# Kernel optimization log

Measured on AMD Instinct MI355X. Metric: run time of the kernel, lower is better.

## Reference

```python
import jax, jax.numpy as jnp
import numpy as np

E, T, D, H = 8, 2048, 1024, 4096  # experts, tokens/expert, model_dim, hidden_size


def setup_inputs() -> dict:
    key = jax.random.key(0)
    k_x, k_w1, k_w2 = jax.random.split(key, 3)
    x = jax.random.normal(k_x, (E, T, D), dtype=jnp.float32)
    fc1_w = jax.random.normal(k_w1, (E, D, H), dtype=jnp.float32) * 0.001
    fc2_w = jax.random.normal(k_w2, (E, H, D), dtype=jnp.float32) * 0.001
    fc1_b = jnp.zeros((E, 1, H), dtype=jnp.float32)
    fc2_b = jnp.zeros((E, 1, D), dtype=jnp.float32)
    return {"x": x, "fc1_w": fc1_w, "fc1_b": fc1_b, "fc2_w": fc2_w, "fc2_b": fc2_b}


def reference(x, fc1_w, fc1_b, fc2_w, fc2_b):
    # batched expert FFN: bmm + bias -> relu -> bmm + bias
    y = jnp.einsum("etd,edh->eth", x, fc1_w) + fc1_b  # [E, T, H]
    y = jax.nn.relu(y)
    y = jnp.einsum("eth,ehd->etd", y, fc2_w) + fc2_b  # [E, T, D]
    return y
```

## Files before the change

kernel.cpp:

```cpp
#include <hip/hip_runtime.h>
#include <hip/hip_bf16.h>
#include <stdint.h>


using frag8 = __attribute__((ext_vector_type(8))) short;
using f32x4 = __attribute__((ext_vector_type(4))) float;

constexpr int E = 8, T = 2048, D = 1024, H = 4096;
constexpr int BM = 256, BN = 256, BK = 64;

__device__ __forceinline__ ushort f2bf(float f) {
    union { float f; uint32_t u; } v; v.f = f;
    return (ushort)((v.u + 0x7FFFu + ((v.u >> 16) & 1u)) >> 16);
}

__device__ __forceinline__ void load16_to_lds(const void* g, void* l) {
    __builtin_amdgcn_global_load_lds(
        (const __attribute__((address_space(1))) uint32_t*)g,
        (__attribute__((address_space(3))) uint32_t*)l, 16, 0, 0);
}


__global__ __launch_bounds__(256) void cvt_bf16_kernel(
    const float* __restrict__ in, ushort* __restrict__ out) {
    const size_t i = ((size_t)blockIdx.x * 256 + threadIdx.x) * 4;
    const float4 v = *(const float4*)(in + i);
    ushort4 o;
    o.x = f2bf(v.x); o.y = f2bf(v.y); o.z = f2bf(v.z); o.w = f2bf(v.w);
    *(ushort4*)(out + i) = o;
}

__global__ __launch_bounds__(256) void transpose_cvt_kernel(
    const float* __restrict__ in, ushort* __restrict__ out, int K, int N) {
    __shared__ __align__(16) ushort tile[64][72];
    const int e = blockIdx.z;
    const int k0 = blockIdx.y * 64, n0 = blockIdx.x * 64;
    const float* ie = in + (size_t)e * K * N + (size_t)k0 * N + n0;
    ushort* oe = out + (size_t)e * N * K + (size_t)n0 * K + k0;
    const int t = threadIdx.x;
    const int lk = t >> 2;
    const int ln = (t & 3) * 16;
#pragma unroll
    for (int v = 0; v < 4; ++v) {
        const float4 f = *(const float4*)(ie + (size_t)lk * N + ln + v * 4);
        tile[ln + v * 4 + 0][lk] = f2bf(f.x);
        tile[ln + v * 4 + 1][lk] = f2bf(f.y);
        tile[ln + v * 4 + 2][lk] = f2bf(f.z);
        tile[ln + v * 4 + 3][lk] = f2bf(f.w);
    }
    __syncthreads();
    const int on = t >> 2;
    const int ok = (t & 3) * 16;
#pragma unroll
    for (int v = 0; v < 2; ++v)
        *(frag8*)(oe + (size_t)on * K + ok + v * 8) = *(const frag8*)&tile[on][ok + v * 8];
}

template <bool RELU_BF16>
__global__ __launch_bounds__(512, 2) void gemm256_kernel(
    const ushort* __restrict__ A, const ushort* __restrict__ Bm,
    const float* __restrict__ bias, void* __restrict__ Cout,
    const int K, const int N) {
    __shared__ __align__(16) char lds[131072];

    const int bid = blockIdx.x;
    const int e = bid & 7;
    const int s = bid >> 3;
    const int m0 = (s & 7) * BM;
    const int n0 = (s >> 3) * BN;

    const ushort* Ae = A + (size_t)e * T * K + (size_t)m0 * K;
    const ushort* Be = Bm + (size_t)e * N * K + (size_t)n0 * K;

    const int tid = threadIdx.x;
    const int lane = tid & 63;
    const int wave = tid >> 6;
    const int wm = wave >> 2;
    const int wn = wave & 3;
    const int col = lane & 15;
    const int quad = lane >> 4;

    const int scc = (lane & 7) ^ (lane >> 3);
    const int srow = wave * 8 + (lane >> 3);
    const ushort* gA0 = Ae + (size_t)srow * K + scc * 8;
    const ushort* gB0 = Be + (size_t)srow * K + scc * 8;
    const int ldsA0 = wave * 1024;
    const int ldsB0 = 32768 + wave * 1024;

    const int swz0 = ((quad ^ (col & 7)) << 4);
    const int swz1 = swz0 ^ 64;
    const int aRow = (wm * 128 + col) * 128;
    const int bRow = (wn * 64 + col) * 128;

    const int NT = K / BK;

#define STAGE_A(p, h, kk) do {                                          \
        const ushort* g_ = gA0 + (size_t)(h) * 128 * K + (kk);          \
        char* l_ = lds + (p) * 65536 + ldsA0 + (h) * 16384;             \
        load16_to_lds(g_, l_);                                          \
        load16_to_lds(g_ + (size_t)64 * K, l_ + 8192);                  \
    } while (0)
#define STAGE_B(p, h, kk) do {                                          \
        const ushort* g_ = gB0 + (size_t)(h) * 128 * K + (kk);          \
        char* l_ = lds + (p) * 65536 + ldsB0 + (h) * 16384;             \
        load16_to_lds(g_, l_);                                          \
        load16_to_lds(g_ + (size_t)64 * K, l_ + 8192);                  \
    } while (0)
#define MFMA(a, b, c) __builtin_amdgcn_mfma_f32_16x16x32_bf16((a), (b), (c), 0, 0, 0)

    f32x4 acc[8][4] = {};
    frag8 A0f[8], A1f[8], Bf[4];

    STAGE_A(0, 0, 0); STAGE_A(0, 1, 0);
    STAGE_B(0, 0, 0); STAGE_B(0, 1, 0);
    STAGE_A(1, 0, BK); STAGE_A(1, 1, BK);
    asm volatile("s_waitcnt vmcnt(4)" ::: "memory");
    __builtin_amdgcn_s_barrier();
    __builtin_amdgcn_sched_barrier(0);

    for (int u = 0; u < NT; ++u) {
        const int p = u & 1, pn = p ^ 1;
        const int kB = (u + 1) * BK;
        const int kA = (u + 2) * BK;
        const bool stB = (u + 1 < NT), stA = (u + 2 < NT);
        const char* aT = lds + p * 65536 + aRow;
        const char* bT = lds + p * 65536 + 32768 + bRow;

#pragma unroll
        for (int i = 0; i < 4; ++i) {
            A0f[i * 2 + 0] = *(const frag8*)(aT + i * 2048 + swz0);
            A0f[i * 2 + 1] = *(const frag8*)(aT + i * 2048 + swz1);
        }
#pragma unroll
        for (int j = 0; j < 2; ++j) {
            Bf[j * 2 + 0] = *(const frag8*)(bT + j * 2048 + swz0);
            Bf[j * 2 + 1] = *(const frag8*)(bT + j * 2048 + swz1);
        }
        if (stB) STAGE_B(pn, 0, kB);
        __builtin_amdgcn_s_barrier();
        asm volatile("s_waitcnt lgkmcnt(0)" ::: "memory");
        __builtin_amdgcn_sched_barrier(0);
        __builtin_amdgcn_s_setprio(1);
#pragma unroll
        for (int i = 0; i < 4; ++i)
#pragma unroll
            for (int j = 0; j < 2; ++j) {
                acc[i][j] = MFMA(A0f[i * 2 + 0], Bf[j * 2 + 0], acc[i][j]);
                acc[i][j] = MFMA(A0f[i * 2 + 1], Bf[j * 2 + 1], acc[i][j]);
            }
        __builtin_amdgcn_s_setprio(0);
        __builtin_amdgcn_s_barrier();
        __builtin_amdgcn_sched_barrier(0);

#pragma unroll
        for (int i = 0; i < 4; ++i) {
            A1f[i * 2 + 0] = *(const frag8*)(aT + 8192 + i * 2048 + swz0);
            A1f[i * 2 + 1] = *(const frag8*)(aT + 8192 + i * 2048 + swz1);
        }
        if (stB) STAGE_B(pn, 1, kB);
        __builtin_amdgcn_s_barrier();
        asm volatile("s_waitcnt lgkmcnt(0)" ::: "memory");
        __builtin_amdgcn_sched_barrier(0);
        __builtin_amdgcn_s_setprio(1);
#pragma unroll
        for (int i = 0; i < 4; ++i)
#pragma unroll
            for (int j = 0; j < 2; ++j) {
                acc[4 + i][j] = MFMA(A1f[i * 2 + 0], Bf[j * 2 + 0], acc[4 + i][j]);
                acc[4 + i][j] = MFMA(A1f[i * 2 + 1], Bf[j * 2 + 1], acc[4 + i][j]);
            }
        __builtin_amdgcn_s_setprio(0);
        __builtin_amdgcn_s_barrier();
        __builtin_amdgcn_sched_barrier(0);

#pragma unroll
        for (int j = 0; j < 2; ++j) {
            Bf[j * 2 + 0] = *(const frag8*)(bT + 4096 + j * 2048 + swz0);
            Bf[j * 2 + 1] = *(const frag8*)(bT + 4096 + j * 2048 + swz1);
        }
        if (stA) STAGE_A(p, 0, kA);
        __builtin_amdgcn_s_barrier();
        asm volatile("s_waitcnt lgkmcnt(0)" ::: "memory");
        __builtin_amdgcn_sched_barrier(0);
        __builtin_amdgcn_s_setprio(1);
#pragma unroll
        for (int i = 0; i < 4; ++i)
#pragma unroll
            for (int j = 0; j < 2; ++j) {
                acc[4 + i][2 + j] = MFMA(A1f[i * 2 + 0], Bf[j * 2 + 0], acc[4 + i][2 + j]);
                acc[4 + i][2 + j] = MFMA(A1f[i * 2 + 1], Bf[j * 2 + 1], acc[4 + i][2 + j]);
            }
        __builtin_amdgcn_s_setprio(0);
        __builtin_amdgcn_s_barrier();
        __builtin_amdgcn_sched_barrier(0);

        if (stA) STAGE_A(p, 1, kA);
        __builtin_amdgcn_s_barrier();
        __builtin_amdgcn_sched_barrier(0);
        __builtin_amdgcn_s_setprio(1);
#pragma unroll
        for (int i = 0; i < 4; ++i)
#pragma unroll
            for (int j = 0; j < 2; ++j) {
                acc[i][2 + j] = MFMA(A0f[i * 2 + 0], Bf[j * 2 + 0], acc[i][2 + j]);
                acc[i][2 + j] = MFMA(A0f[i * 2 + 1], Bf[j * 2 + 1], acc[i][2 + j]);
            }
        __builtin_amdgcn_s_setprio(0);
        if (stA) {
            asm volatile("s_waitcnt vmcnt(4)" ::: "memory");
        } else if (stB) {
            asm volatile("s_waitcnt vmcnt(0)" ::: "memory");
        }
        __builtin_amdgcn_s_barrier();
        __builtin_amdgcn_sched_barrier(0);
    }

    const float* be = bias + (size_t)e * N;
#pragma unroll
    for (int j = 0; j < 4; ++j) {
        const int nn = n0 + wn * 64 + j * 16 + col;
        const float bv = be[nn];
#pragma unroll
        for (int i = 0; i < 8; ++i) {
            const int mb = m0 + wm * 128 + i * 16 + quad * 4;
#pragma unroll
            for (int r = 0; r < 4; ++r) {
                float v = acc[i][j][r] + bv;
                if (RELU_BF16) {
                    v = v > 0.f ? v : 0.f;
                    ((ushort*)Cout)[(size_t)e * T * N + (size_t)(mb + r) * N + nn] = f2bf(v);
                } else {
                    ((float*)Cout)[(size_t)e * T * N + (size_t)(mb + r) * N + nn] = v;
                }
            }
        }
    }
#undef STAGE_A
#undef STAGE_B
#undef MFMA
}


constexpr int FBM = 128, FBN = 128, FBK = 32;
constexpr int FLDK = FBK + 16;

__global__ __launch_bounds__(256) void fb_gemm1_kernel(
    const float* __restrict__ x, const float* __restrict__ w1,
    const float* __restrict__ b1, ushort* __restrict__ y1) {
    __shared__ __align__(16) ushort As[FBM * FLDK];
    __shared__ __align__(16) ushort Bs[FBN * FLDK];
    const int e = blockIdx.z, m0 = blockIdx.y * FBM, n0 = blockIdx.x * FBN;
    const float* xa = x + (size_t)e * T * D + (size_t)m0 * D;
    const float* wb = w1 + (size_t)e * D * H;
    const int tid = threadIdx.x, lane = tid & 63, wave = tid >> 6;
    const int waveM = (wave >> 1) * 64, waveN = (wave & 1) * 64;
    const int col = lane & 15, quad = lane >> 4;
    const int ar = tid >> 3, ak = (tid & 7) * 4;
    const int bn = tid & 127, bk = (tid >> 7) * 16;
    f32x4 acc[4][4] = {};
    for (int k0 = 0; k0 < D; k0 += FBK) {
#pragma unroll
        for (int p = 0; p < 4; ++p) {
            const float4 v = *(const float4*)(xa + (size_t)(ar + 32 * p) * D + k0 + ak);
            ushort* dst = &As[(ar + 32 * p) * FLDK + ak];
            dst[0] = f2bf(v.x); dst[1] = f2bf(v.y); dst[2] = f2bf(v.z); dst[3] = f2bf(v.w);
        }
        {
            ushort tmp[16];
#pragma unroll
            for (int j = 0; j < 16; ++j)
                tmp[j] = f2bf(wb[(size_t)(k0 + bk + j) * H + n0 + bn]);
            ushort* dst = &Bs[bn * FLDK + bk];
#pragma unroll
            for (int j = 0; j < 16; ++j) dst[j] = tmp[j];
        }
        __syncthreads();
        frag8 af[4], bf[4];
#pragma unroll
        for (int i = 0; i < 4; ++i) {
            af[i] = *(const frag8*)&As[(waveM + i * 16 + col) * FLDK + quad * 8];
            bf[i] = *(const frag8*)&Bs[(waveN + i * 16 + col) * FLDK + quad * 8];
        }
#pragma unroll
        for (int i = 0; i < 4; ++i)
#pragma unroll
            for (int j = 0; j < 4; ++j)
                acc[i][j] = __builtin_amdgcn_mfma_f32_16x16x32_bf16(af[i], bf[j], acc[i][j], 0, 0, 0);
        __syncthreads();
    }
    const float* be = b1 + (size_t)e * H;
    ushort* ye = y1 + (size_t)e * T * H;
#pragma unroll
    for (int j = 0; j < 4; ++j) {
        const int n = n0 + waveN + j * 16 + col;
        const float bias = be[n];
#pragma unroll
        for (int i = 0; i < 4; ++i) {
            const int mb = m0 + waveM + i * 16 + quad * 4;
#pragma unroll
            for (int r = 0; r < 4; ++r) {
                float v = acc[i][j][r] + bias;
                v = v > 0.f ? v : 0.f;
                ye[(size_t)(mb + r) * H + n] = f2bf(v);
            }
        }
    }
}

__global__ __launch_bounds__(256) void fb_gemm2_kernel(
    const ushort* __restrict__ y1, const float* __restrict__ w2,
    const float* __restrict__ b2, float* __restrict__ out) {
    __shared__ __align__(16) ushort As[FBM * FLDK];
    __shared__ __align__(16) ushort Bs[FBN * FLDK];
    const int e = blockIdx.z, m0 = blockIdx.y * FBM, n0 = blockIdx.x * FBN;
    const ushort* ya = y1 + (size_t)e * T * H + (size_t)m0 * H;
    const float* wb = w2 + (size_t)e * H * D;
    const int tid = threadIdx.x, lane = tid & 63, wave = tid >> 6;
    const int waveM = (wave >> 1) * 64, waveN = (wave & 1) * 64;
    const int col = lane & 15, quad = lane >> 4;
    const int ar = tid >> 2, ak = (tid & 3) * 8;
    const int bn = tid & 127, bk = (tid >> 7) * 16;
    f32x4 acc[4][4] = {};
    for (int k0 = 0; k0 < H; k0 += FBK) {
#pragma unroll
        for (int p = 0; p < 2; ++p)
            *(frag8*)&As[(ar + 64 * p) * FLDK + ak] =
                *(const frag8*)(ya + (size_t)(ar + 64 * p) * H + k0 + ak);
        {
            ushort tmp[16];
#pragma unroll
            for (int j = 0; j < 16; ++j)
                tmp[j] = f2bf(wb[(size_t)(k0 + bk + j) * D + n0 + bn]);
            ushort* dst = &Bs[bn * FLDK + bk];
#pragma unroll
            for (int j = 0; j < 16; ++j) dst[j] = tmp[j];
        }
        __syncthreads();
        frag8 af[4], bf[4];
#pragma unroll
        for (int i = 0; i < 4; ++i) {
            af[i] = *(const frag8*)&As[(waveM + i * 16 + col) * FLDK + quad * 8];
            bf[i] = *(const frag8*)&Bs[(waveN + i * 16 + col) * FLDK + quad * 8];
        }
#pragma unroll
        for (int i = 0; i < 4; ++i)
#pragma unroll
            for (int j = 0; j < 4; ++j)
                acc[i][j] = __builtin_amdgcn_mfma_f32_16x16x32_bf16(af[i], bf[j], acc[i][j], 0, 0, 0);
        __syncthreads();
    }
    const float* be = b2 + (size_t)e * D;
    float* oe = out + (size_t)e * T * D;
#pragma unroll
    for (int j = 0; j < 4; ++j) {
        const int n = n0 + waveN + j * 16 + col;
        const float bias = be[n];
#pragma unroll
        for (int i = 0; i < 4; ++i) {
            const int mb = m0 + waveM + i * 16 + quad * 4;
#pragma unroll
            for (int r = 0; r < 4; ++r)
                oe[(size_t)(mb + r) * D + n] = acc[i][j][r] + bias;
        }
    }
}

extern "C" void kernel_launch(void* const* d_in, const int* in_sizes, int n_in,
                              void* d_out, int out_size, void* d_ws, size_t ws_size,
                              hipStream_t stream) {
    const float* x  = (const float*)d_in[0];
    const float* w1 = (const float*)d_in[1];
    const float* b1 = (const float*)d_in[2];
    const float* w2 = (const float*)d_in[3];
    const float* b2 = (const float*)d_in[4];
    float* out = (float*)d_out;

    const size_t y1_bytes = (size_t)E * T * H * 2;
    const size_t wt_bytes = (size_t)E * D * H * 2;
    const size_t xb_bytes = (size_t)E * T * D * 2;
    const size_t need = y1_bytes + wt_bytes + xb_bytes;

    if (ws_size >= need) {
        ushort* y1 = (ushort*)d_ws;
        ushort* wt = (ushort*)((char*)d_ws + y1_bytes);
        ushort* xb = (ushort*)((char*)d_ws + y1_bytes + wt_bytes);

        cvt_bf16_kernel<<<(E * T * D) / (256 * 4), 256, 0, stream>>>(x, xb);
        transpose_cvt_kernel<<<dim3(H / 64, D / 64, E), 256, 0, stream>>>(w1, wt, D, H);
        gemm256_kernel<true><<<E * (T / BM) * (H / BN), 512, 0, stream>>>(xb, wt, b1, y1, D, H);
        transpose_cvt_kernel<<<dim3(D / 64, H / 64, E), 256, 0, stream>>>(w2, wt, H, D);
        gemm256_kernel<false><<<E * (T / BM) * (D / BN), 512, 0, stream>>>(y1, wt, b2, out, H, D);
    } else {
        ushort* y1 = (ushort*)d_ws;
        fb_gemm1_kernel<<<dim3(H / FBN, T / FBM, E), 256, 0, stream>>>(x, w1, b1, y1);
        fb_gemm2_kernel<<<dim3(D / FBN, T / FBM, E), 256, 0, stream>>>(y1, w2, b2, out);
    }
}
```

Baseline: 640.8 us.

## Interleave warp sub-tiles across halves and reorder B/A staging with unrolled ping-pong loop

Each wave's 128x64 output region now comes from two 64-row blocks of A that sit 128 rows apart and two 32-column blocks of B that sit 128 columns apart, so every sub-tile read reaches into both staged halves of LDS. The staging schedule also changes: B half 1 of the next tile is issued first, then A halves, and B half 0 is prefetched into the current buffer one tile ahead, which raises the outstanding load count to 6. The main loop is unrolled by two with constant buffer indices. The aim is to let each staged half be consumed and overwritten earlier, giving more overlap between global loads and MFMA work, at the cost of more in-flight loads and a trickier WAR ordering.

```diff
diff --git a/kernel.cpp b/kernel.cpp
--- a/kernel.cpp
+++ b/kernel.cpp
@@ -89,8 +89,8 @@
 
     const int swz0 = ((quad ^ (col & 7)) << 4);
     const int swz1 = swz0 ^ 64;
-    const int aRow = (wm * 128 + col) * 128;
-    const int bRow = (wn * 64 + col) * 128;
+    const int aRow = (wm * 64 + col) * 128;
+    const int bRow = (wn * 32 + col) * 128;
 
     const int NT = K / BK;
 
@@ -113,116 +113,119 @@
 
     STAGE_A(0, 0, 0); STAGE_A(0, 1, 0);
     STAGE_B(0, 0, 0); STAGE_B(0, 1, 0);
-    STAGE_A(1, 0, BK); STAGE_A(1, 1, BK);
-    asm volatile("s_waitcnt vmcnt(4)" ::: "memory");
+    STAGE_A(1, 0, BK); STAGE_A(1, 1, BK); STAGE_B(1, 0, BK);
+    asm volatile("s_waitcnt vmcnt(6)" ::: "memory");
     __builtin_amdgcn_s_barrier();
     __builtin_amdgcn_sched_barrier(0);
 
-    for (int u = 0; u < NT; ++u) {
-        const int p = u & 1, pn = p ^ 1;
-        const int kB = (u + 1) * BK;
-        const int kA = (u + 2) * BK;
-        const bool stB = (u + 1 < NT), stA = (u + 2 < NT);
-        const char* aT = lds + p * 65536 + aRow;
-        const char* bT = lds + p * 65536 + 32768 + bRow;
-
-#pragma unroll
-        for (int i = 0; i < 4; ++i) {
-            A0f[i * 2 + 0] = *(const frag8*)(aT + i * 2048 + swz0);
-            A0f[i * 2 + 1] = *(const frag8*)(aT + i * 2048 + swz1);
-        }
-#pragma unroll
-        for (int j = 0; j < 2; ++j) {
-            Bf[j * 2 + 0] = *(const frag8*)(bT + j * 2048 + swz0);
-            Bf[j * 2 + 1] = *(const frag8*)(bT + j * 2048 + swz1);
-        }
-        if (stB) STAGE_B(pn, 0, kB);
-        __builtin_amdgcn_s_barrier();
-        asm volatile("s_waitcnt lgkmcnt(0)" ::: "memory");
-        __builtin_amdgcn_sched_barrier(0);
-        __builtin_amdgcn_s_setprio(1);
-#pragma unroll
-        for (int i = 0; i < 4; ++i)
-#pragma unroll
-            for (int j = 0; j < 2; ++j) {
-                acc[i][j] = MFMA(A0f[i * 2 + 0], Bf[j * 2 + 0], acc[i][j]);
-                acc[i][j] = MFMA(A0f[i * 2 + 1], Bf[j * 2 + 1], acc[i][j]);
-            }
-        __builtin_amdgcn_s_setprio(0);
-        __builtin_amdgcn_s_barrier();
-        __builtin_amdgcn_sched_barrier(0);
-
-#pragma unroll
-        for (int i = 0; i < 4; ++i) {
-            A1f[i * 2 + 0] = *(const frag8*)(aT + 8192 + i * 2048 + swz0);
-            A1f[i * 2 + 1] = *(const frag8*)(aT + 8192 + i * 2048 + swz1);
-        }
-        if (stB) STAGE_B(pn, 1, kB);
-        __builtin_amdgcn_s_barrier();
-        asm volatile("s_waitcnt lgkmcnt(0)" ::: "memory");
-        __builtin_amdgcn_sched_barrier(0);
-        __builtin_amdgcn_s_setprio(1);
-#pragma unroll
-        for (int i = 0; i < 4; ++i)
-#pragma unroll
-            for (int j = 0; j < 2; ++j) {
-                acc[4 + i][j] = MFMA(A1f[i * 2 + 0], Bf[j * 2 + 0], acc[4 + i][j]);
-                acc[4 + i][j] = MFMA(A1f[i * 2 + 1], Bf[j * 2 + 1], acc[4 + i][j]);
-            }
-        __builtin_amdgcn_s_setprio(0);
-        __builtin_amdgcn_s_barrier();
-        __builtin_amdgcn_sched_barrier(0);
-
-#pragma unroll
-        for (int j = 0; j < 2; ++j) {
-            Bf[j * 2 + 0] = *(const frag8*)(bT + 4096 + j * 2048 + swz0);
-            Bf[j * 2 + 1] = *(const frag8*)(bT + 4096 + j * 2048 + swz1);
-        }
-        if (stA) STAGE_A(p, 0, kA);
-        __builtin_amdgcn_s_barrier();
-        asm volatile("s_waitcnt lgkmcnt(0)" ::: "memory");
-        __builtin_amdgcn_sched_barrier(0);
-        __builtin_amdgcn_s_setprio(1);
-#pragma unroll
-        for (int i = 0; i < 4; ++i)
-#pragma unroll
-            for (int j = 0; j < 2; ++j) {
-                acc[4 + i][2 + j] = MFMA(A1f[i * 2 + 0], Bf[j * 2 + 0], acc[4 + i][2 + j]);
-                acc[4 + i][2 + j] = MFMA(A1f[i * 2 + 1], Bf[j * 2 + 1], acc[4 + i][2 + j]);
-            }
-        __builtin_amdgcn_s_setprio(0);
-        __builtin_amdgcn_s_barrier();
-        __builtin_amdgcn_sched_barrier(0);
-
-        if (stA) STAGE_A(p, 1, kA);
-        __builtin_amdgcn_s_barrier();
-        __builtin_amdgcn_sched_barrier(0);
-        __builtin_amdgcn_s_setprio(1);
-#pragma unroll
-        for (int i = 0; i < 4; ++i)
-#pragma unroll
-            for (int j = 0; j < 2; ++j) {
-                acc[i][2 + j] = MFMA(A0f[i * 2 + 0], Bf[j * 2 + 0], acc[i][2 + j]);
-                acc[i][2 + j] = MFMA(A0f[i * 2 + 1], Bf[j * 2 + 1], acc[i][2 + j]);
-            }
-        __builtin_amdgcn_s_setprio(0);
-        if (stA) {
-            asm volatile("s_waitcnt vmcnt(4)" ::: "memory");
-        } else if (stB) {
-            asm volatile("s_waitcnt vmcnt(0)" ::: "memory");
-        }
-        __builtin_amdgcn_s_barrier();
-        __builtin_amdgcn_sched_barrier(0);
-    }
+#define TILE_ITER(u, p, pn) do {                                              \
+        const int kB_ = ((u) + 1) * BK, kA_ = ((u) + 2) * BK;                 \
+        const bool stB_ = (u) + 1 < NT, stA_ = (u) + 2 < NT;                  \
+        const char* aT = lds + (p) * 65536 + aRow;                            \
+        const char* bT = lds + (p) * 65536 + 32768 + bRow;                    \
+                        \
+        _Pragma("unroll")                                                     \
+        for (int i = 0; i < 4; ++i) {                                         \
+            A0f[i * 2 + 0] = *(const frag8*)(aT + i * 2048 + swz0);           \
+            A0f[i * 2 + 1] = *(const frag8*)(aT + i * 2048 + swz1);           \
+        }                                                                     \
+        _Pragma("unroll")                                                     \
+        for (int j = 0; j < 2; ++j) {                                         \
+            Bf[j * 2 + 0] = *(const frag8*)(bT + j * 2048 + swz0);            \
+            Bf[j * 2 + 1] = *(const frag8*)(bT + j * 2048 + swz1);            \
+        }                                                                     \
+        if (stB_) STAGE_B(pn, 1, kB_);                                        \
+        __builtin_amdgcn_s_barrier();                                         \
+        asm volatile("s_waitcnt lgkmcnt(0)" ::: "memory");                    \
+        __builtin_amdgcn_sched_barrier(0);                                    \
+        __builtin_amdgcn_s_setprio(1);                                        \
+        _Pragma("unroll")                                                     \
+        for (int i = 0; i < 4; ++i)                                           \
+            _Pragma("unroll")                                                 \
+            for (int j = 0; j < 2; ++j) {                                     \
+                acc[i][j] = MFMA(A0f[i * 2 + 0], Bf[j * 2 + 0], acc[i][j]);   \
+                acc[i][j] = MFMA(A0f[i * 2 + 1], Bf[j * 2 + 1], acc[i][j]);   \
+            }                                                                 \
+        __builtin_amdgcn_s_setprio(0);                                        \
+        __builtin_amdgcn_s_barrier();                                         \
+        __builtin_amdgcn_sched_barrier(0);                                    \
+        \
+        _Pragma("unroll")                                                     \
+        for (int i = 0; i < 4; ++i) {                                         \
+            A1f[i * 2 + 0] = *(const frag8*)(aT + 16384 + i * 2048 + swz0);   \
+            A1f[i * 2 + 1] = *(const frag8*)(aT + 16384 + i * 2048 + swz1);   \
+        }                                                                     \
+        if (stA_) STAGE_A(p, 0, kA_);                                         \
+        __builtin_amdgcn_s_barrier();                                         \
+        asm volatile("s_waitcnt lgkmcnt(0)" ::: "memory");                    \
+        __builtin_amdgcn_sched_barrier(0);                                    \
+        __builtin_amdgcn_s_setprio(1);                                        \
+        _Pragma("unroll")                                                     \
+        for (int i = 0; i < 4; ++i)                                           \
+            _Pragma("unroll")                                                 \
+            for (int j = 0; j < 2; ++j) {                                     \
+                acc[4 + i][j] = MFMA(A1f[i * 2 + 0], Bf[j * 2 + 0], acc[4 + i][j]); \
+                acc[4 + i][j] = MFMA(A1f[i * 2 + 1], Bf[j * 2 + 1], acc[4 + i][j]); \
+            }                                                                 \
+        __builtin_amdgcn_s_setprio(0);                                        \
+        __builtin_amdgcn_s_barrier();                                         \
+        __builtin_amdgcn_sched_barrier(0);                                    \
+        \
+        _Pragma("unroll")                                                     \
+        for (int j = 0; j < 2; ++j) {                                         \
+            Bf[j * 2 + 0] = *(const frag8*)(bT + 16384 + j * 2048 + swz0);    \
+            Bf[j * 2 + 1] = *(const frag8*)(bT + 16384 + j * 2048 + swz1);    \
+        }                                                                     \
+        if (stA_) STAGE_A(p, 1, kA_);                                         \
+        __builtin_amdgcn_s_barrier();                                         \
+        asm volatile("s_waitcnt lgkmcnt(0)" ::: "memory");                    \
+        __builtin_amdgcn_sched_barrier(0);                                    \
+        __builtin_amdgcn_s_setprio(1);                                        \
+        _Pragma("unroll")                                                     \
+        for (int i = 0; i < 4; ++i)                                           \
+            _Pragma("unroll")                                                 \
+            for (int j = 0; j < 2; ++j) {                                     \
+                acc[4 + i][2 + j] = MFMA(A1f[i * 2 + 0], Bf[j * 2 + 0], acc[4 + i][2 + j]); \
+                acc[4 + i][2 + j] = MFMA(A1f[i * 2 + 1], Bf[j * 2 + 1], acc[4 + i][2 + j]); \
+            }                                                                 \
+        __builtin_amdgcn_s_setprio(0);                                        \
+        __builtin_amdgcn_s_barrier();                                         \
+        __builtin_amdgcn_sched_barrier(0);                                    \
+        \
+        if (stA_) STAGE_B(p, 0, kA_);                                         \
+        __builtin_amdgcn_s_setprio(1);                                        \
+        _Pragma("unroll")                                                     \
+        for (int i = 0; i < 4; ++i)                                           \
+            _Pragma("unroll")                                                 \
+            for (int j = 0; j < 2; ++j) {                                     \
+                acc[i][2 + j] = MFMA(A0f[i * 2 + 0], Bf[j * 2 + 0], acc[i][2 + j]); \
+                acc[i][2 + j] = MFMA(A0f[i * 2 + 1], Bf[j * 2 + 1], acc[i][2 + j]); \
+            }                                                                 \
+        __builtin_amdgcn_s_setprio(0);                                        \
+             \
+        if (stA_) {                                                           \
+            asm volatile("s_waitcnt vmcnt(6)" ::: "memory");                  \
+        } else if (stB_) {                                                    \
+            asm volatile("s_waitcnt vmcnt(0)" ::: "memory");                  \
+        }                                                                     \
+        __builtin_amdgcn_s_barrier();                                         \
+        __builtin_amdgcn_sched_barrier(0);                                    \
+    } while (0)
+
+    for (int v = 0; v < NT / 2; ++v) {
+        TILE_ITER(2 * v, 0, 1);
+        TILE_ITER(2 * v + 1, 1, 0);
+    }
+#undef TILE_ITER
 
     const float* be = bias + (size_t)e * N;
 #pragma unroll
     for (int j = 0; j < 4; ++j) {
-        const int nn = n0 + wn * 64 + j * 16 + col;
+        const int nn = n0 + wn * 32 + (j & 1) * 16 + (j >> 1) * 128 + col;
         const float bv = be[nn];
 #pragma unroll
         for (int i = 0; i < 8; ++i) {
-            const int mb = m0 + wm * 128 + i * 16 + quad * 4;
+            const int mb = m0 + wm * 64 + (i & 3) * 16 + (i >> 2) * 128 + quad * 4;
 #pragma unroll
             for (int r = 0; r < 4; ++r) {
                 float v = acc[i][j][r] + bv;
```

After: 602.0 us. -6.1%, faster.
